# Performance work log

Measured on AMD Instinct MI355X. Metric: run time of the kernel, lower is better.

## Reference

```python
import jax, jax.numpy as jnp
import numpy as np

NUM_HEADS = 4


def setup_inputs() -> dict:
    key = jax.random.key(0)
    ks = jax.random.split(key, 5)
    B, N, D = 4096, 49, 128  # B = batch(64) * num_windows(64), N = 7*7 window
    nW = 64
    x = jax.random.normal(ks[0], (B, N, D), dtype=jnp.float32)
    mask = jax.random.normal(ks[1], (nW, N, N), dtype=jnp.float32)
    w_qkv = jax.random.normal(ks[2], (3 * D, D), dtype=jnp.float32) * 0.02
    w_proj = jax.random.normal(ks[3], (D, D), dtype=jnp.float32) * 0.02
    b_proj = jax.random.normal(ks[4], (D,), dtype=jnp.float32) * 0.02
    return {"x": x, "mask": mask, "w_qkv": w_qkv, "w_proj": w_proj, "b_proj": b_proj}


def reference(x, mask, w_qkv, w_proj, b_proj):
    B, N, D = x.shape
    H = NUM_HEADS
    hd = D // H
    scale = hd ** (-0.5)
    # qkv projection (torch Linear: y = x @ W^T), no bias
    qkv = (x @ w_qkv.T).reshape(B, N, 3, H, hd)
    qkv = jnp.transpose(qkv, (2, 0, 3, 1, 4))  # [3, B, H, N, hd]
    q, k, v = qkv[0], qkv[1], qkv[2]
    attn = jnp.einsum("bhqd,bhkd->bhqk", q, k) * scale  # [B, H, N, N]
    nW = mask.shape[0]
    # add per-window additive mask, broadcast over batch and heads
    attn = attn.reshape(B // nW, nW, H, N, N) + mask[None, :, None, :, :]
    attn = attn.reshape(B, H, N, N)
    attn = jax.nn.softmax(attn, axis=-1)
    out = jnp.einsum("bhqk,bhkd->bhqd", attn, v)  # [B, H, N, hd]
    out = jnp.transpose(out, (0, 2, 1, 3)).reshape(B, N, D)
    return out @ w_proj.T + b_proj
```

## Files before the change

kernel.cpp:

```cpp
#include <hip/hip_runtime.h>
#include <hip/hip_bf16.h>

typedef _Float16 f16;
typedef __attribute__((ext_vector_type(8))) _Float16 f16x8;
typedef __attribute__((ext_vector_type(4))) _Float16 f16x4;
typedef __attribute__((ext_vector_type(4))) float f32x4;

#define MFMA16(a, b, c) __builtin_amdgcn_mfma_f32_16x16x32_f16((a), (b), (c), 0, 0, 0)

#define NWIN 4096
#define WPB 16

__global__ void cvt_weights(const float* __restrict__ wq,
                            const float* __restrict__ wp,
                            f16* __restrict__ o) {
    int i = blockIdx.x * blockDim.x + threadIdx.x;
    if (i < 49152) o[i] = (f16)wq[i];
    if (i < 16384) o[49152 + i] = (f16)wp[i];
}

__device__ inline f16x8 cvt8(const float* p) {
    float4 u0 = *(const float4*)p;
    float4 u1 = *(const float4*)(p + 4);
    f16x8 t;
    t[0] = (f16)u0.x; t[1] = (f16)u0.y; t[2] = (f16)u0.z; t[3] = (f16)u0.w;
    t[4] = (f16)u1.x; t[5] = (f16)u1.y; t[6] = (f16)u1.z; t[7] = (f16)u1.w;
    return t;
}

__global__ __launch_bounds__(512, 1)
void fused_all(const float* __restrict__ x, const float* __restrict__ mask,
               const f16* __restrict__ wq_h, const f16* __restrict__ wp_h,
               const float* __restrict__ bias, float* __restrict__ out) {
    __shared__ f16 xb[2][50 * 128];
    __shared__ f16 qlds[2][64 * 128];
    __shared__ f16 klds[2][64 * 128];
    __shared__ f16 vlds[2][128 * 64];
    __shared__ f16 scr[8][2048];

    const int tid = threadIdx.x;
    const int wave = tid >> 6;
    const int lane = tid & 63;
    const int lg = lane >> 4;
    const int lr = lane & 15;
    const int w0 = blockIdx.x * WPB;

    const int amt = wave & 3;
    const int ahh = wave >> 2;
    const int ar0 = amt * 16;

    f16* ps0 = scr[wave];
    f16* ps1 = scr[wave] + 1024;

    f16x8 bw[3][4];
#pragma unroll
    for (int j = 0; j < 3; ++j)
#pragma unroll
        for (int kc = 0; kc < 4; ++kc)
            bw[j][kc] = *(const f16x8*)&wq_h[((wave + 8 * j) * 16 + lr) * 128 + kc * 32 + 8 * lg];
    f16x8 wpr[4];
#pragma unroll
    for (int kc = 0; kc < 4; ++kc)
        wpr[kc] = *(const f16x8*)&wp_h[(wave * 16 + lr) * 128 + kc * 32 + 8 * lg];
    const float4 bcv = *(const float4*)&bias[wave * 16 + 4 * lg];

    auto stage = [&](int w, int p) {
        const float* xw = x + (size_t)w * (49 * 128);
        for (int i = tid; i < 1568; i += 512) {
            const int row = i >> 5;
            const int c4 = (i & 31) << 2;
            float4 v = ((const float4*)xw)[i];
            f16x4 t;
            t[0] = (f16)v.x; t[1] = (f16)v.y; t[2] = (f16)v.z; t[3] = (f16)v.w;
            *(f16x4*)&xb[p][row * 128 + (c4 ^ ((row & 7) << 3))] = t;
        }
    };

    stage(w0, 0);
    __syncthreads();

    const float sc = 0.17677669529663687f;

    for (int wi = 0; wi < WPB; ++wi) {
        const int w = w0 + wi;
        const int cur = wi & 1;
        if (wi < WPB - 1) stage(w + 1, cur ^ 1);

        const float* mw = mask + (size_t)(w & 63) * (49 * 49);
        const int qrow = ar0 + lr;
        float mv[4][4];
#pragma unroll
        for (int reg = 0; reg < 4; ++reg) {
#pragma unroll
            for (int nt = 0; nt < 4; ++nt) {
                const int k = 4 * lg + reg + 16 * nt;
                mv[reg][nt] = (qrow < 49 && k < 49) ? mw[qrow * 49 + k] : 0.f;
            }
        }

        f16* ql = qlds[cur];
        f16* kl = klds[cur];
        f16* vl = vlds[cur];
#pragma unroll
        for (int mt = 0; mt < 4; ++mt) {
            const int nb = mt * 16;
            const int xrow = nb + lr;
            f16x8 a[4];
            if (xrow < 49) {
#pragma unroll
                for (int kc = 0; kc < 4; ++kc)
                    a[kc] = *(const f16x8*)&xb[cur][xrow * 128 + ((kc * 32 + 8 * lg) ^ ((xrow & 7) << 3))];
            } else {
                f16x8 z = {0, 0, 0, 0, 0, 0, 0, 0};
#pragma unroll
                for (int kc = 0; kc < 4; ++kc) a[kc] = z;
            }

#pragma unroll
            for (int j = 0; j < 2; ++j) {
                __builtin_amdgcn_s_setprio(1);
                f32x4 acc = {0.f, 0.f, 0.f, 0.f};
#pragma unroll
                for (int kc = 0; kc < 4; ++kc) acc = MFMA16(bw[j][kc], a[kc], acc);
                __builtin_amdgcn_s_setprio(0);

                const int n = nb + lr;
                const int cb = wave * 16 + 4 * lg;
                f16x4 t;
#pragma unroll
                for (int reg = 0; reg < 4; ++reg) t[reg] = (f16)acc[reg];
                f16* dst = (j == 0) ? ql : kl;
                *(f16x4*)&dst[n * 128 + (cb ^ ((n & 7) << 3))] = t;
            }
            {
                __builtin_amdgcn_s_setprio(1);
                f32x4 acc = {0.f, 0.f, 0.f, 0.f};
#pragma unroll
                for (int kc = 0; kc < 4; ++kc) acc = MFMA16(a[kc], bw[2][kc], acc);
                __builtin_amdgcn_s_setprio(0);

                const int c = wave * 16 + lr;
                f16x4 t;
#pragma unroll
                for (int reg = 0; reg < 4; ++reg) t[reg] = (f16)acc[reg];
                *(f16x4*)&vl[c * 64 + ((nb + 4 * lg) ^ ((c & 7) << 3))] = t;
            }
        }
        __syncthreads();

        const int h0 = 2 * ahh;
        const int h1 = 2 * ahh + 1;

        f16x8 aq0 = *(const f16x8*)&ql[qrow * 128 + ((h0 * 32 + 8 * lg) ^ ((qrow & 7) << 3))];
        f16x8 aq1 = *(const f16x8*)&ql[qrow * 128 + ((h1 * 32 + 8 * lg) ^ ((qrow & 7) << 3))];

        f32x4 s0[4], s1[4];
        {
            __builtin_amdgcn_s_setprio(1);
#pragma unroll
            for (int nt = 0; nt < 4; ++nt) {
                const int krow = nt * 16 + lr;
                f16x8 bk = *(const f16x8*)&kl[krow * 128 + ((h0 * 32 + 8 * lg) ^ ((krow & 7) << 3))];
                f32x4 z = {0.f, 0.f, 0.f, 0.f};
                s0[nt] = MFMA16(bk, aq0, z);
            }
#pragma unroll
            for (int nt = 0; nt < 4; ++nt) {
                const int krow = nt * 16 + lr;
                f16x8 bk = *(const f16x8*)&kl[krow * 128 + ((h1 * 32 + 8 * lg) ^ ((krow & 7) << 3))];
                f32x4 z = {0.f, 0.f, 0.f, 0.f};
                s1[nt] = MFMA16(bk, aq1, z);
            }
            __builtin_amdgcn_s_setprio(0);
        }

        float sum0 = 0.f, sum1 = 0.f;
#pragma unroll
        for (int nt = 0; nt < 4; ++nt) {
            f16x4 p0t, p1t;
#pragma unroll
            for (int reg = 0; reg < 4; ++reg) {
                const int k = 4 * lg + reg + 16 * nt;
                float e0 = (k < 49) ? __expf(s0[nt][reg] * sc + mv[reg][nt]) : 0.f;
                float e1 = (k < 49) ? __expf(s1[nt][reg] * sc + mv[reg][nt]) : 0.f;
                sum0 += e0;
                sum1 += e1;
                p0t[reg] = (f16)e0;
                p1t[reg] = (f16)e1;
            }
            const int off = lr * 64 + ((4 * lg + 16 * nt) ^ ((lr & 7) << 3));
            *(f16x4*)&ps0[off] = p0t;
            *(f16x4*)&ps1[off] = p1t;
        }
        sum0 += __shfl_xor(sum0, 16, 64);
        sum0 += __shfl_xor(sum0, 32, 64);
        sum1 += __shfl_xor(sum1, 16, 64);
        sum1 += __shfl_xor(sum1, 32, 64);
        const float inv0 = __fdividef(1.f, sum0);
        const float inv1 = __fdividef(1.f, sum1);

        f16x8 bv0[2][2], bv1[2][2];
#pragma unroll
        for (int nt = 0; nt < 2; ++nt)
#pragma unroll
            for (int kc = 0; kc < 2; ++kc) {
                const int vr0 = h0 * 32 + nt * 16 + lr;
                const int vr1 = h1 * 32 + nt * 16 + lr;
                bv0[nt][kc] = *(const f16x8*)&vl[vr0 * 64 + ((kc * 32 + 8 * lg) ^ ((vr0 & 7) << 3))];
                bv1[nt][kc] = *(const f16x8*)&vl[vr1 * 64 + ((kc * 32 + 8 * lg) ^ ((vr1 & 7) << 3))];
            }

        f16x8 ap0[2], ap1[2];
#pragma unroll
        for (int kc = 0; kc < 2; ++kc) {
            const int off = lr * 64 + ((kc * 32 + 8 * lg) ^ ((lr & 7) << 3));
            ap0[kc] = *(const f16x8*)&ps0[off];
            ap1[kc] = *(const f16x8*)&ps1[off];
        }
        f32x4 o00 = {0.f, 0.f, 0.f, 0.f}, o01 = {0.f, 0.f, 0.f, 0.f};
        f32x4 o10 = {0.f, 0.f, 0.f, 0.f}, o11 = {0.f, 0.f, 0.f, 0.f};
        __builtin_amdgcn_s_setprio(1);
#pragma unroll
        for (int kc = 0; kc < 2; ++kc) {
            o00 = MFMA16(bv0[0][kc], ap0[kc], o00);
            o01 = MFMA16(bv0[1][kc], ap0[kc], o01);
            o10 = MFMA16(bv1[0][kc], ap1[kc], o10);
            o11 = MFMA16(bv1[1][kc], ap1[kc], o11);
        }
        __builtin_amdgcn_s_setprio(0);

#pragma unroll
        for (int reg = 0; reg < 4; ++reg) {
            o00[reg] *= inv0;
            o01[reg] *= inv0;
            o10[reg] *= inv1;
            o11[reg] *= inv1;
        }

        {
            const int n = ar0 + lr;
            const int s = (n & 7) << 3;
            f16x4 t;
#pragma unroll
            for (int reg = 0; reg < 4; ++reg) t[reg] = (f16)o00[reg];
            *(f16x4*)&ql[n * 128 + ((h0 * 32 + 4 * lg) ^ s)] = t;
#pragma unroll
            for (int reg = 0; reg < 4; ++reg) t[reg] = (f16)o01[reg];
            *(f16x4*)&ql[n * 128 + ((h0 * 32 + 16 + 4 * lg) ^ s)] = t;
#pragma unroll
            for (int reg = 0; reg < 4; ++reg) t[reg] = (f16)o10[reg];
            *(f16x4*)&ql[n * 128 + ((h1 * 32 + 4 * lg) ^ s)] = t;
#pragma unroll
            for (int reg = 0; reg < 4; ++reg) t[reg] = (f16)o11[reg];
            *(f16x4*)&ql[n * 128 + ((h1 * 32 + 16 + 4 * lg) ^ s)] = t;
        }
        __syncthreads();

        float* ob = out + (size_t)w * (49 * 128);
#pragma unroll
        for (int mt = 0; mt < 4; ++mt) {
            const int prow = mt * 16 + lr;
            f16x8 aa[4];
#pragma unroll
            for (int kc = 0; kc < 4; ++kc)
                aa[kc] = *(const f16x8*)&ql[prow * 128 + ((kc * 32 + 8 * lg) ^ ((prow & 7) << 3))];
            __builtin_amdgcn_s_setprio(1);
            f32x4 acc = {0.f, 0.f, 0.f, 0.f};
#pragma unroll
            for (int kc = 0; kc < 4; ++kc) acc = MFMA16(wpr[kc], aa[kc], acc);
            __builtin_amdgcn_s_setprio(0);

            if (prow < 49) {
                float4 o;
                o.x = acc[0] + bcv.x;
                o.y = acc[1] + bcv.y;
                o.z = acc[2] + bcv.z;
                o.w = acc[3] + bcv.w;
                *(float4*)&ob[prow * 128 + wave * 16 + 4 * lg] = o;
            }
        }
    }
}

template <bool WB>
__global__ __launch_bounds__(256, 4)
void fused_wattn(const float* __restrict__ x, const float* __restrict__ mask,
                 const float* __restrict__ wq_f, const float* __restrict__ wp_f,
                 const f16* __restrict__ wq_h, const f16* __restrict__ wp_h,
                 const float* __restrict__ bias, float* __restrict__ out) {
    __shared__ f16 ks[64 * 128];
    __shared__ f16 vt[128 * 64];
    __shared__ f16 scr[4][1024];

    const int b = blockIdx.x;
    const int wid = b & 63;
    const int tid = threadIdx.x;
    const int wave = tid >> 6;
    const int lane = tid & 63;
    const int lg = lane >> 4;
    const int lr = lane & 15;
    const int r0 = wave * 16;
    f16* ps = scr[wave];

    f16x8 a[4];
    {
        const int xrow = r0 + lr;
        if (xrow < 49) {
            const float* xp = x + ((size_t)b * 49 + xrow) * 128 + 8 * lg;
#pragma unroll
            for (int kc = 0; kc < 4; ++kc) a[kc] = cvt8(xp + kc * 32);
        } else {
            f16x8 z = {0, 0, 0, 0, 0, 0, 0, 0};
#pragma unroll
            for (int kc = 0; kc < 4; ++kc) a[kc] = z;
        }
    }

    float mv[4][4];
#pragma unroll
    for (int reg = 0; reg < 4; ++reg) {
        const int n = r0 + 4 * lg + reg;
#pragma unroll
        for (int nt = 0; nt < 4; ++nt) {
            const int col = nt * 16 + lr;
            mv[reg][nt] = (n < 49 && col < 49) ? mask[((size_t)wid * 49 + n) * 49 + col] : 0.f;
        }
    }

    f16x4 qd[8];
#pragma unroll
    for (int ct = 0; ct < 24; ++ct) {
        const int wrow = ct * 16 + lr;
        f16x8 bw[4];
        if (WB) {
#pragma unroll
            for (int kc = 0; kc < 4; ++kc)
                bw[kc] = *(const f16x8*)&wq_h[wrow * 128 + kc * 32 + 8 * lg];
        } else {
#pragma unroll
            for (int kc = 0; kc < 4; ++kc)
                bw[kc] = cvt8(&wq_f[wrow * 128 + kc * 32 + 8 * lg]);
        }
        f32x4 acc = {0.f, 0.f, 0.f, 0.f};
#pragma unroll
        for (int kc = 0; kc < 4; ++kc) acc = MFMA16(a[kc], bw[kc], acc);

        if (ct < 8) {
            f16x4 q;
#pragma unroll
            for (int reg = 0; reg < 4; ++reg) q[reg] = (f16)acc[reg];
            qd[ct] = q;
        } else if (ct < 16) {
#pragma unroll
            for (int reg = 0; reg < 4; ++reg) {
                const int n = r0 + 4 * lg + reg;
                const int c = wrow - 128;
                ks[n * 128 + (c ^ ((n & 7) << 3))] = (f16)acc[reg];
            }
        } else {
#pragma unroll
            for (int reg = 0; reg < 4; ++reg) {
                const int n = r0 + 4 * lg + reg;
                const int dch = wrow - 256;
                vt[dch * 64 + (n ^ ((dch & 7) << 3))] = (f16)acc[reg];
            }
        }
    }
    __syncthreads();

    const float sc = 0.17677669529663687f;
    f32x4 oacc[4][2];

#pragma unroll
    for (int h = 0; h < 4; ++h) {
#pragma unroll
        for (int c2 = 0; c2 < 2; ++c2)
#pragma unroll
            for (int reg = 0; reg < 4; ++reg) {
                const int row = 4 * lg + reg;
                const int col = c2 * 16 + lr;
                ps[row * 32 + (col ^ ((row & 3) << 3))] = qd[2 * h + c2][reg];
            }
        f16x8 aq = *(const f16x8*)&ps[lr * 32 + ((8 * lg) ^ ((lr & 3) << 3))];

        f32x4 s[4];
#pragma unroll
        for (int nt = 0; nt < 4; ++nt) {
            const int krow = nt * 16 + lr;
            f16x8 bk = *(const f16x8*)&ks[krow * 128 + ((h * 32 + 8 * lg) ^ ((krow & 7) << 3))];
            f32x4 z = {0.f, 0.f, 0.f, 0.f};
            s[nt] = MFMA16(aq, bk, z);
        }

#pragma unroll
        for (int reg = 0; reg < 4; ++reg) {
            float vals[4];
            float sum = 0.f;
#pragma unroll
            for (int nt = 0; nt < 4; ++nt) {
                const int col = nt * 16 + lr;
                float e = (col < 49) ? __expf(s[nt][reg] * sc + mv[reg][nt]) : 0.f;
                vals[nt] = e;
                sum += e;
            }
            for (int d = 1; d < 16; d <<= 1) sum += __shfl_xor(sum, d, 64);
            const float inv = __fdividef(1.f, sum);
            const int row = 4 * lg + reg;
#pragma unroll
            for (int nt = 0; nt < 4; ++nt) {
                const int col = nt * 16 + lr;
                ps[row * 64 + (col ^ ((row & 7) << 3))] = (f16)(vals[nt] * inv);
            }
        }

        f16x8 ap[2];
#pragma unroll
        for (int kc = 0; kc < 2; ++kc)
            ap[kc] = *(const f16x8*)&ps[lr * 64 + ((kc * 32 + 8 * lg) ^ ((lr & 7) << 3))];
#pragma unroll
        for (int nt = 0; nt < 2; ++nt) {
            const int vrow = h * 32 + nt * 16 + lr;
            f32x4 acc = {0.f, 0.f, 0.f, 0.f};
#pragma unroll
            for (int kc = 0; kc < 2; ++kc) {
                f16x8 bv = *(const f16x8*)&vt[vrow * 64 + ((kc * 32 + 8 * lg) ^ ((vrow & 7) << 3))];
                acc = MFMA16(ap[kc], bv, acc);
            }
            oacc[h][nt] = acc;
        }
    }

    f16x8 aa[4];
#pragma unroll
    for (int pass = 0; pass < 2; ++pass) {
#pragma unroll
        for (int h2 = 0; h2 < 2; ++h2)
#pragma unroll
            for (int nt = 0; nt < 2; ++nt)
#pragma unroll
                for (int reg = 0; reg < 4; ++reg) {
                    const int row = 4 * lg + reg;
                    const int col = h2 * 32 + nt * 16 + lr;
                    ps[row * 64 + (col ^ ((row & 7) << 3))] = (f16)oacc[pass * 2 + h2][nt][reg];
                }
#pragma unroll
        for (int kcg = 0; kcg < 2; ++kcg)
            aa[pass * 2 + kcg] = *(const f16x8*)&ps[lr * 64 + ((kcg * 32 + 8 * lg) ^ ((lr & 7) << 3))];
    }

    float* ob = out + (size_t)b * (49 * 128);
#pragma unroll
    for (int ct = 0; ct < 8; ++ct) {
        const int wrow = ct * 16 + lr;
        f16x8 bw[4];
        if (WB) {
#pragma unroll
            for (int kc = 0; kc < 4; ++kc)
                bw[kc] = *(const f16x8*)&wp_h[wrow * 128 + kc * 32 + 8 * lg];
        } else {
#pragma unroll
            for (int kc = 0; kc < 4; ++kc)
                bw[kc] = cvt8(&wp_f[wrow * 128 + kc * 32 + 8 * lg]);
        }
        f32x4 acc = {0.f, 0.f, 0.f, 0.f};
#pragma unroll
        for (int kc = 0; kc < 4; ++kc) acc = MFMA16(aa[kc], bw[kc], acc);

        const float bc = bias[wrow];
#pragma unroll
        for (int reg = 0; reg < 4; ++reg) {
            const int n = r0 + 4 * lg + reg;
            if (n < 49) ob[n * 128 + ct * 16 + lr] = acc[reg] + bc;
        }
    }
}

extern "C" void kernel_launch(void* const* d_in, const int* in_sizes, int n_in,
                              void* d_out, int out_size, void* d_ws, size_t ws_size,
                              hipStream_t stream) {
    const float* x = (const float*)d_in[0];
    const float* mask = (const float*)d_in[1];
    const float* wq = (const float*)d_in[2];
    const float* wp = (const float*)d_in[3];
    const float* bp = (const float*)d_in[4];
    float* out = (float*)d_out;

    const size_t need_wb = (size_t)(49152 + 16384) * sizeof(f16);

    if (ws_size >= need_wb && d_ws != nullptr) {
        f16* wsh = (f16*)d_ws;
        cvt_weights<<<192, 256, 0, stream>>>(wq, wp, wsh);
        fused_all<<<NWIN / WPB, 512, 0, stream>>>(x, mask, wsh, wsh + 49152, bp, out);
    } else {
        fused_wattn<false><<<4096, 256, 0, stream>>>(x, mask, wq, wp, nullptr, nullptr, bp, out);
    }
}
```

Baseline: 98.11 us.

## Split 1024-thread block into two halves processing interleaved windows concurrently

The fused attention kernel now runs 1024 threads per block as two independent 512-thread halves, each owning one of the previously double-buffered LDS sets and processing alternating windows. This replaces the old software prefetch (stage next window into the other buffer) with staging issued after the QKV sync, and the per-head attention is processed sequentially to shrink register pressure and scratch. The aim is more resident waves to hide latency, at the cost of block-wide barriers coupling both halves and an extra barrier per iteration.

```diff
diff --git a/kernel.cpp b/kernel.cpp
--- a/kernel.cpp
+++ b/kernel.cpp
@@ -9,7 +9,7 @@
 #define MFMA16(a, b, c) __builtin_amdgcn_mfma_f32_16x16x32_f16((a), (b), (c), 0, 0, 0)
 
 #define NWIN 4096
-#define WPB 16
+#define WPH 8
 
 __global__ void cvt_weights(const float* __restrict__ wq,
                             const float* __restrict__ wp,
@@ -28,7 +28,7 @@
     return t;
 }
 
-__global__ __launch_bounds__(512, 1)
+__global__ __launch_bounds__(1024, 1)
 void fused_all(const float* __restrict__ x, const float* __restrict__ mask,
                const f16* __restrict__ wq_h, const f16* __restrict__ wp_h,
                const float* __restrict__ bias, float* __restrict__ out) {
@@ -36,55 +36,55 @@
     __shared__ f16 qlds[2][64 * 128];
     __shared__ f16 klds[2][64 * 128];
     __shared__ f16 vlds[2][128 * 64];
-    __shared__ f16 scr[8][2048];
+    __shared__ f16 scr[16][1024];
 
     const int tid = threadIdx.x;
     const int wave = tid >> 6;
+    const int half = wave >> 3;
+    const int hw = wave & 7;
+    const int ltid = tid & 511;
     const int lane = tid & 63;
     const int lg = lane >> 4;
     const int lr = lane & 15;
-    const int w0 = blockIdx.x * WPB;
-
-    const int amt = wave & 3;
-    const int ahh = wave >> 2;
+    const int w0 = blockIdx.x * (2 * WPH);
+
+    const int amt = hw & 3;
+    const int ahh = hw >> 2;
     const int ar0 = amt * 16;
 
-    f16* ps0 = scr[wave];
-    f16* ps1 = scr[wave] + 1024;
+    f16* ps = scr[wave];
 
     f16x8 bw[3][4];
 #pragma unroll
     for (int j = 0; j < 3; ++j)
 #pragma unroll
         for (int kc = 0; kc < 4; ++kc)
-            bw[j][kc] = *(const f16x8*)&wq_h[((wave + 8 * j) * 16 + lr) * 128 + kc * 32 + 8 * lg];
+            bw[j][kc] = *(const f16x8*)&wq_h[((hw + 8 * j) * 16 + lr) * 128 + kc * 32 + 8 * lg];
     f16x8 wpr[4];
 #pragma unroll
     for (int kc = 0; kc < 4; ++kc)
-        wpr[kc] = *(const f16x8*)&wp_h[(wave * 16 + lr) * 128 + kc * 32 + 8 * lg];
-    const float4 bcv = *(const float4*)&bias[wave * 16 + 4 * lg];
-
-    auto stage = [&](int w, int p) {
+        wpr[kc] = *(const f16x8*)&wp_h[(hw * 16 + lr) * 128 + kc * 32 + 8 * lg];
+    const float4 bcv = *(const float4*)&bias[hw * 16 + 4 * lg];
+
+    auto stage = [&](int w) {
         const float* xw = x + (size_t)w * (49 * 128);
-        for (int i = tid; i < 1568; i += 512) {
+        for (int i = ltid; i < 1568; i += 512) {
             const int row = i >> 5;
             const int c4 = (i & 31) << 2;
             float4 v = ((const float4*)xw)[i];
             f16x4 t;
             t[0] = (f16)v.x; t[1] = (f16)v.y; t[2] = (f16)v.z; t[3] = (f16)v.w;
-            *(f16x4*)&xb[p][row * 128 + (c4 ^ ((row & 7) << 3))] = t;
+            *(f16x4*)&xb[half][row * 128 + (c4 ^ ((row & 7) << 3))] = t;
         }
     };
 
-    stage(w0, 0);
+    stage(w0 + half);
     __syncthreads();
 
     const float sc = 0.17677669529663687f;
 
-    for (int wi = 0; wi < WPB; ++wi) {
-        const int w = w0 + wi;
-        const int cur = wi & 1;
-        if (wi < WPB - 1) stage(w + 1, cur ^ 1);
+    for (int wi = 0; wi < WPH; ++wi) {
+        const int w = w0 + 2 * wi + half;
 
         const float* mw = mask + (size_t)(w & 63) * (49 * 49);
         const int qrow = ar0 + lr;
@@ -98,9 +98,9 @@
             }
         }
 
-        f16* ql = qlds[cur];
-        f16* kl = klds[cur];
-        f16* vl = vlds[cur];
+        f16* ql = qlds[half];
+        f16* kl = klds[half];
+        f16* vl = vlds[half];
 #pragma unroll
         for (int mt = 0; mt < 4; ++mt) {
             const int nb = mt * 16;
@@ -109,7 +109,7 @@
             if (xrow < 49) {
 #pragma unroll
                 for (int kc = 0; kc < 4; ++kc)
-                    a[kc] = *(const f16x8*)&xb[cur][xrow * 128 + ((kc * 32 + 8 * lg) ^ ((xrow & 7) << 3))];
+                    a[kc] = *(const f16x8*)&xb[half][xrow * 128 + ((kc * 32 + 8 * lg) ^ ((xrow & 7) << 3))];
             } else {
                 f16x8 z = {0, 0, 0, 0, 0, 0, 0, 0};
 #pragma unroll
@@ -125,7 +125,7 @@
                 __builtin_amdgcn_s_setprio(0);
 
                 const int n = nb + lr;
-                const int cb = wave * 16 + 4 * lg;
+                const int cb = hw * 16 + 4 * lg;
                 f16x4 t;
 #pragma unroll
                 for (int reg = 0; reg < 4; ++reg) t[reg] = (f16)acc[reg];
@@ -139,7 +139,7 @@
                 for (int kc = 0; kc < 4; ++kc) acc = MFMA16(a[kc], bw[2][kc], acc);
                 __builtin_amdgcn_s_setprio(0);
 
-                const int c = wave * 16 + lr;
+                const int c = hw * 16 + lr;
                 f16x4 t;
 #pragma unroll
                 for (int reg = 0; reg < 4; ++reg) t[reg] = (f16)acc[reg];
@@ -148,96 +148,85 @@
         }
         __syncthreads();
 
-        const int h0 = 2 * ahh;
-        const int h1 = 2 * ahh + 1;
-
-        f16x8 aq0 = *(const f16x8*)&ql[qrow * 128 + ((h0 * 32 + 8 * lg) ^ ((qrow & 7) << 3))];
-        f16x8 aq1 = *(const f16x8*)&ql[qrow * 128 + ((h1 * 32 + 8 * lg) ^ ((qrow & 7) << 3))];
-
-        f32x4 s0[4], s1[4];
-        {
+        if (wi + 1 < WPH) stage(w + 2);
+
+        f32x4 o00, o01, o10, o11;
+#pragma unroll
+        for (int hi = 0; hi < 2; ++hi) {
+            const int h = 2 * ahh + hi;
+            f16x8 aq = *(const f16x8*)&ql[qrow * 128 + ((h * 32 + 8 * lg) ^ ((qrow & 7) << 3))];
+
+            f32x4 s[4];
             __builtin_amdgcn_s_setprio(1);
 #pragma unroll
             for (int nt = 0; nt < 4; ++nt) {
                 const int krow = nt * 16 + lr;
-                f16x8 bk = *(const f16x8*)&kl[krow * 128 + ((h0 * 32 + 8 * lg) ^ ((krow & 7) << 3))];
+                f16x8 bk = *(const f16x8*)&kl[krow * 128 + ((h * 32 + 8 * lg) ^ ((krow & 7) << 3))];
                 f32x4 z = {0.f, 0.f, 0.f, 0.f};
-                s0[nt] = MFMA16(bk, aq0, z);
-            }
+                s[nt] = MFMA16(bk, aq, z);
+            }
+            __builtin_amdgcn_s_setprio(0);
+
+            float sum = 0.f;
 #pragma unroll
             for (int nt = 0; nt < 4; ++nt) {
-                const int krow = nt * 16 + lr;
-                f16x8 bk = *(const f16x8*)&kl[krow * 128 + ((h1 * 32 + 8 * lg) ^ ((krow & 7) << 3))];
-                f32x4 z = {0.f, 0.f, 0.f, 0.f};
-                s1[nt] = MFMA16(bk, aq1, z);
+                f16x4 pt;
+#pragma unroll
+                for (int reg = 0; reg < 4; ++reg) {
+                    const int k = 4 * lg + reg + 16 * nt;
+                    float e = (k < 49) ? __expf(s[nt][reg] * sc + mv[reg][nt]) : 0.f;
+                    sum += e;
+                    pt[reg] = (f16)e;
+                }
+                const int off = lr * 64 + ((4 * lg + 16 * nt) ^ ((lr & 7) << 3));
+                *(f16x4*)&ps[off] = pt;
+            }
+            sum += __shfl_xor(sum, 16, 64);
+            sum += __shfl_xor(sum, 32, 64);
+            const float inv = __fdividef(1.f, sum);
+
+            f16x8 bv[2][2];
+#pragma unroll
+            for (int nt = 0; nt < 2; ++nt)
+#pragma unroll
+                for (int kc = 0; kc < 2; ++kc) {
+                    const int vr = h * 32 + nt * 16 + lr;
+                    bv[nt][kc] = *(const f16x8*)&vl[vr * 64 + ((kc * 32 + 8 * lg) ^ ((vr & 7) << 3))];
+                }
+
+            f16x8 ap[2];
+#pragma unroll
+            for (int kc = 0; kc < 2; ++kc) {
+                const int off = lr * 64 + ((kc * 32 + 8 * lg) ^ ((lr & 7) << 3));
+                ap[kc] = *(const f16x8*)&ps[off];
+            }
+            f32x4 oa = {0.f, 0.f, 0.f, 0.f};
+            f32x4 ob_ = {0.f, 0.f, 0.f, 0.f};
+            __builtin_amdgcn_s_setprio(1);
+#pragma unroll
+            for (int kc = 0; kc < 2; ++kc) {
+                oa = MFMA16(bv[0][kc], ap[kc], oa);
+                ob_ = MFMA16(bv[1][kc], ap[kc], ob_);
             }
             __builtin_amdgcn_s_setprio(0);
-        }
-
-        float sum0 = 0.f, sum1 = 0.f;
-#pragma unroll
-        for (int nt = 0; nt < 4; ++nt) {
-            f16x4 p0t, p1t;
+
 #pragma unroll
             for (int reg = 0; reg < 4; ++reg) {
-                const int k = 4 * lg + reg + 16 * nt;
-                float e0 = (k < 49) ? __expf(s0[nt][reg] * sc + mv[reg][nt]) : 0.f;
-                float e1 = (k < 49) ? __expf(s1[nt][reg] * sc + mv[reg][nt]) : 0.f;
-                sum0 += e0;
-                sum1 += e1;
-                p0t[reg] = (f16)e0;
-                p1t[reg] = (f16)e1;
-            }
-            const int off = lr * 64 + ((4 * lg + 16 * nt) ^ ((lr & 7) << 3));
-            *(f16x4*)&ps0[off] = p0t;
-            *(f16x4*)&ps1[off] = p1t;
-        }
-        sum0 += __shfl_xor(sum0, 16, 64);
-        sum0 += __shfl_xor(sum0, 32, 64);
-        sum1 += __shfl_xor(sum1, 16, 64);
-        sum1 += __shfl_xor(sum1, 32, 64);
-        const float inv0 = __fdividef(1.f, sum0);
-        const float inv1 = __fdividef(1.f, sum1);
-
-        f16x8 bv0[2][2], bv1[2][2];
-#pragma unroll
-        for (int nt = 0; nt < 2; ++nt)
-#pragma unroll
-            for (int kc = 0; kc < 2; ++kc) {
-                const int vr0 = h0 * 32 + nt * 16 + lr;
-                const int vr1 = h1 * 32 + nt * 16 + lr;
-                bv0[nt][kc] = *(const f16x8*)&vl[vr0 * 64 + ((kc * 32 + 8 * lg) ^ ((vr0 & 7) << 3))];
-                bv1[nt][kc] = *(const f16x8*)&vl[vr1 * 64 + ((kc * 32 + 8 * lg) ^ ((vr1 & 7) << 3))];
-            }
-
-        f16x8 ap0[2], ap1[2];
-#pragma unroll
-        for (int kc = 0; kc < 2; ++kc) {
-            const int off = lr * 64 + ((kc * 32 + 8 * lg) ^ ((lr & 7) << 3));
-            ap0[kc] = *(const f16x8*)&ps0[off];
-            ap1[kc] = *(const f16x8*)&ps1[off];
-        }
-        f32x4 o00 = {0.f, 0.f, 0.f, 0.f}, o01 = {0.f, 0.f, 0.f, 0.f};
-        f32x4 o10 = {0.f, 0.f, 0.f, 0.f}, o11 = {0.f, 0.f, 0.f, 0.f};
-        __builtin_amdgcn_s_setprio(1);
-#pragma unroll
-        for (int kc = 0; kc < 2; ++kc) {
-            o00 = MFMA16(bv0[0][kc], ap0[kc], o00);
-            o01 = MFMA16(bv0[1][kc], ap0[kc], o01);
-            o10 = MFMA16(bv1[0][kc], ap1[kc], o10);
-            o11 = MFMA16(bv1[1][kc], ap1[kc], o11);
-        }
-        __builtin_amdgcn_s_setprio(0);
-
-#pragma unroll
-        for (int reg = 0; reg < 4; ++reg) {
-            o00[reg] *= inv0;
-            o01[reg] *= inv0;
-            o10[reg] *= inv1;
-            o11[reg] *= inv1;
+                oa[reg] *= inv;
+                ob_[reg] *= inv;
+            }
+            if (hi == 0) {
+                o00 = oa;
+                o01 = ob_;
+            } else {
+                o10 = oa;
+                o11 = ob_;
+            }
         }
 
         {
+            const int h0 = 2 * ahh;
+            const int h1 = 2 * ahh + 1;
             const int n = ar0 + lr;
             const int s = (n & 7) << 3;
             f16x4 t;
@@ -276,9 +265,10 @@
                 o.y = acc[1] + bcv.y;
                 o.z = acc[2] + bcv.z;
                 o.w = acc[3] + bcv.w;
-                *(float4*)&ob[prow * 128 + wave * 16 + 4 * lg] = o;
-            }
-        }
+                *(float4*)&ob[prow * 128 + hw * 16 + 4 * lg] = o;
+            }
+        }
+        __syncthreads();
     }
 }
 
@@ -490,7 +480,7 @@
     if (ws_size >= need_wb && d_ws != nullptr) {
         f16* wsh = (f16*)d_ws;
         cvt_weights<<<192, 256, 0, stream>>>(wq, wp, wsh);
-        fused_all<<<NWIN / WPB, 512, 0, stream>>>(x, mask, wsh, wsh + 49152, bp, out);
+        fused_all<<<NWIN / (2 * WPH), 1024, 0, stream>>>(x, mask, wsh, wsh + 49152, bp, out);
     } else {
         fused_wattn<false><<<4096, 256, 0, stream>>>(x, mask, wq, wp, nullptr, nullptr, bp, out);
     }
```

Measured after the change: 217.9 us. 122% more time.

## Process windows in pairs per phase to halve block barriers

Applied to the files above, without the earlier changes.

The persistent kernel now handles two windows per iteration. It runs QKV projection for both, syncs, stages the next two windows' x, runs attention for both, syncs, then runs the output projection for both. This cuts barriers per window and lets more independent work sit between them. It also replaces the per-element k<49 select in the softmax with a -1e30 mask bias. In exchange, prefetch of x is now serialized after the first barrier rather than overlapped with QKV, and a third barrier per pair is added.

```diff
diff --git a/kernel.cpp b/kernel.cpp
--- a/kernel.cpp
+++ b/kernel.cpp
@@ -48,6 +48,7 @@
     const int amt = wave & 3;
     const int ahh = wave >> 2;
     const int ar0 = amt * 16;
+    const int qrow = ar0 + lr;
 
     f16* ps0 = scr[wave];
     f16* ps1 = scr[wave] + 1024;
@@ -77,85 +78,98 @@
     };
 
     stage(w0, 0);
+    stage(w0 + 1, 1);
     __syncthreads();
 
     const float sc = 0.17677669529663687f;
 
-    for (int wi = 0; wi < WPB; ++wi) {
-        const int w = w0 + wi;
-        const int cur = wi & 1;
-        if (wi < WPB - 1) stage(w + 1, cur ^ 1);
-
-        const float* mw = mask + (size_t)(w & 63) * (49 * 49);
-        const int qrow = ar0 + lr;
-        float mv[4][4];
-#pragma unroll
-        for (int reg = 0; reg < 4; ++reg) {
-#pragma unroll
-            for (int nt = 0; nt < 4; ++nt) {
-                const int k = 4 * lg + reg + 16 * nt;
-                mv[reg][nt] = (qrow < 49 && k < 49) ? mw[qrow * 49 + k] : 0.f;
-            }
-        }
-
-        f16* ql = qlds[cur];
-        f16* kl = klds[cur];
-        f16* vl = vlds[cur];
-#pragma unroll
-        for (int mt = 0; mt < 4; ++mt) {
-            const int nb = mt * 16;
-            const int xrow = nb + lr;
-            f16x8 a[4];
-            if (xrow < 49) {
-#pragma unroll
-                for (int kc = 0; kc < 4; ++kc)
-                    a[kc] = *(const f16x8*)&xb[cur][xrow * 128 + ((kc * 32 + 8 * lg) ^ ((xrow & 7) << 3))];
-            } else {
-                f16x8 z = {0, 0, 0, 0, 0, 0, 0, 0};
-#pragma unroll
-                for (int kc = 0; kc < 4; ++kc) a[kc] = z;
-            }
-
-#pragma unroll
-            for (int j = 0; j < 2; ++j) {
-                __builtin_amdgcn_s_setprio(1);
-                f32x4 acc = {0.f, 0.f, 0.f, 0.f};
-#pragma unroll
-                for (int kc = 0; kc < 4; ++kc) acc = MFMA16(bw[j][kc], a[kc], acc);
-                __builtin_amdgcn_s_setprio(0);
-
-                const int n = nb + lr;
-                const int cb = wave * 16 + 4 * lg;
-                f16x4 t;
-#pragma unroll
-                for (int reg = 0; reg < 4; ++reg) t[reg] = (f16)acc[reg];
-                f16* dst = (j == 0) ? ql : kl;
-                *(f16x4*)&dst[n * 128 + (cb ^ ((n & 7) << 3))] = t;
-            }
-            {
-                __builtin_amdgcn_s_setprio(1);
-                f32x4 acc = {0.f, 0.f, 0.f, 0.f};
-#pragma unroll
-                for (int kc = 0; kc < 4; ++kc) acc = MFMA16(a[kc], bw[2][kc], acc);
-                __builtin_amdgcn_s_setprio(0);
-
-                const int c = wave * 16 + lr;
-                f16x4 t;
-#pragma unroll
-                for (int reg = 0; reg < 4; ++reg) t[reg] = (f16)acc[reg];
-                *(f16x4*)&vl[c * 64 + ((nb + 4 * lg) ^ ((c & 7) << 3))] = t;
+    for (int pi = 0; pi < WPB / 2; ++pi) {
+        const int wA = w0 + 2 * pi;
+
+#pragma unroll
+        for (int ws = 0; ws < 2; ++ws) {
+            f16* ql = qlds[ws];
+            f16* kl = klds[ws];
+            f16* vl = vlds[ws];
+#pragma unroll
+            for (int mt = 0; mt < 4; ++mt) {
+                const int nb = mt * 16;
+                const int xrow = nb + lr;
+                f16x8 a[4];
+                if (xrow < 49) {
+#pragma unroll
+                    for (int kc = 0; kc < 4; ++kc)
+                        a[kc] = *(const f16x8*)&xb[ws][xrow * 128 + ((kc * 32 + 8 * lg) ^ ((xrow & 7) << 3))];
+                } else {
+                    f16x8 z = {0, 0, 0, 0, 0, 0, 0, 0};
+#pragma unroll
+                    for (int kc = 0; kc < 4; ++kc) a[kc] = z;
+                }
+
+#pragma unroll
+                for (int j = 0; j < 2; ++j) {
+                    __builtin_amdgcn_s_setprio(1);
+                    f32x4 acc = {0.f, 0.f, 0.f, 0.f};
+#pragma unroll
+                    for (int kc = 0; kc < 4; ++kc) acc = MFMA16(bw[j][kc], a[kc], acc);
+                    __builtin_amdgcn_s_setprio(0);
+
+                    const int n = nb + lr;
+                    const int cb = wave * 16 + 4 * lg;
+                    f16x4 t;
+#pragma unroll
+                    for (int reg = 0; reg < 4; ++reg) t[reg] = (f16)acc[reg];
+                    f16* dst = (j == 0) ? ql : kl;
+                    *(f16x4*)&dst[n * 128 + (cb ^ ((n & 7) << 3))] = t;
+                }
+                {
+                    __builtin_amdgcn_s_setprio(1);
+                    f32x4 acc = {0.f, 0.f, 0.f, 0.f};
+#pragma unroll
+                    for (int kc = 0; kc < 4; ++kc) acc = MFMA16(a[kc], bw[2][kc], acc);
+                    __builtin_amdgcn_s_setprio(0);
+
+                    const int c = wave * 16 + lr;
+                    f16x4 t;
+#pragma unroll
+                    for (int reg = 0; reg < 4; ++reg) t[reg] = (f16)acc[reg];
+                    *(f16x4*)&vl[c * 64 + ((nb + 4 * lg) ^ ((c & 7) << 3))] = t;
+                }
             }
         }
         __syncthreads();
 
-        const int h0 = 2 * ahh;
-        const int h1 = 2 * ahh + 1;
-
-        f16x8 aq0 = *(const f16x8*)&ql[qrow * 128 + ((h0 * 32 + 8 * lg) ^ ((qrow & 7) << 3))];
-        f16x8 aq1 = *(const f16x8*)&ql[qrow * 128 + ((h1 * 32 + 8 * lg) ^ ((qrow & 7) << 3))];
-
-        f32x4 s0[4], s1[4];
-        {
+        if (pi + 1 < WPB / 2) {
+            stage(wA + 2, 0);
+            stage(wA + 3, 1);
+        }
+
+#pragma unroll
+        for (int ws = 0; ws < 2; ++ws) {
+            const int w = wA + ws;
+            f16* ql = qlds[ws];
+            f16* kl = klds[ws];
+            f16* vl = vlds[ws];
+
+            const int h0 = 2 * ahh;
+            const int h1 = 2 * ahh + 1;
+
+            const float* mw = mask + (size_t)(w & 63) * (49 * 49);
+            float mv[4][4];
+#pragma unroll
+            for (int reg = 0; reg < 4; ++reg) {
+#pragma unroll
+                for (int nt = 0; nt < 4; ++nt) {
+                    const int k = 4 * lg + reg + 16 * nt;
+                    mv[reg][nt] = (k >= 49) ? -1e30f
+                                  : (qrow < 49) ? mw[qrow * 49 + k] : 0.f;
+                }
+            }
+
+            f16x8 aq0 = *(const f16x8*)&ql[qrow * 128 + ((h0 * 32 + 8 * lg) ^ ((qrow & 7) << 3))];
+            f16x8 aq1 = *(const f16x8*)&ql[qrow * 128 + ((h1 * 32 + 8 * lg) ^ ((qrow & 7) << 3))];
+
+            f32x4 s0[4], s1[4];
             __builtin_amdgcn_s_setprio(1);
 #pragma unroll
             for (int nt = 0; nt < 4; ++nt) {
@@ -172,113 +186,109 @@
                 s1[nt] = MFMA16(bk, aq1, z);
             }
             __builtin_amdgcn_s_setprio(0);
-        }
-
-        float sum0 = 0.f, sum1 = 0.f;
-#pragma unroll
-        for (int nt = 0; nt < 4; ++nt) {
-            f16x4 p0t, p1t;
-#pragma unroll
-            for (int reg = 0; reg < 4; ++reg) {
-                const int k = 4 * lg + reg + 16 * nt;
-                float e0 = (k < 49) ? __expf(s0[nt][reg] * sc + mv[reg][nt]) : 0.f;
-                float e1 = (k < 49) ? __expf(s1[nt][reg] * sc + mv[reg][nt]) : 0.f;
-                sum0 += e0;
-                sum1 += e1;
-                p0t[reg] = (f16)e0;
-                p1t[reg] = (f16)e1;
-            }
-            const int off = lr * 64 + ((4 * lg + 16 * nt) ^ ((lr & 7) << 3));
-            *(f16x4*)&ps0[off] = p0t;
-            *(f16x4*)&ps1[off] = p1t;
-        }
-        sum0 += __shfl_xor(sum0, 16, 64);
-        sum0 += __shfl_xor(sum0, 32, 64);
-        sum1 += __shfl_xor(sum1, 16, 64);
-        sum1 += __shfl_xor(sum1, 32, 64);
-        const float inv0 = __fdividef(1.f, sum0);
-        const float inv1 = __fdividef(1.f, sum1);
-
-        f16x8 bv0[2][2], bv1[2][2];
-#pragma unroll
-        for (int nt = 0; nt < 2; ++nt)
+
+            float sum0 = 0.f, sum1 = 0.f;
+#pragma unroll
+            for (int nt = 0; nt < 4; ++nt) {
+                f16x4 p0t, p1t;
+#pragma unroll
+                for (int reg = 0; reg < 4; ++reg) {
+                    float e0 = __expf(s0[nt][reg] * sc + mv[reg][nt]);
+                    float e1 = __expf(s1[nt][reg] * sc + mv[reg][nt]);
+                    sum0 += e0;
+                    sum1 += e1;
+                    p0t[reg] = (f16)e0;
+                    p1t[reg] = (f16)e1;
+                }
+                const int off = lr * 64 + ((4 * lg + 16 * nt) ^ ((lr & 7) << 3));
+                *(f16x4*)&ps0[off] = p0t;
+                *(f16x4*)&ps1[off] = p1t;
+            }
+            sum0 += __shfl_xor(sum0, 16, 64);
+            sum0 += __shfl_xor(sum0, 32, 64);
+            sum1 += __shfl_xor(sum1, 16, 64);
+            sum1 += __shfl_xor(sum1, 32, 64);
+            const float inv0 = __fdividef(1.f, sum0);
+            const float inv1 = __fdividef(1.f, sum1);
+
+            f16x8 bv0[2][2], bv1[2][2];
+#pragma unroll
+            for (int nt = 0; nt < 2; ++nt)
+#pragma unroll
+                for (int kc = 0; kc < 2; ++kc) {
+                    const int vr0 = h0 * 32 + nt * 16 + lr;
+                    const int vr1 = h1 * 32 + nt * 16 + lr;
+                    bv0[nt][kc] = *(const f16x8*)&vl[vr0 * 64 + ((kc * 32 + 8 * lg) ^ ((vr0 & 7) << 3))];
+                    bv1[nt][kc] = *(const f16x8*)&vl[vr1 * 64 + ((kc * 32 + 8 * lg) ^ ((vr1 & 7) << 3))];
+                }
+
+            f16x8 ap0[2], ap1[2];
 #pragma unroll
             for (int kc = 0; kc < 2; ++kc) {
-                const int vr0 = h0 * 32 + nt * 16 + lr;
-                const int vr1 = h1 * 32 + nt * 16 + lr;
-                bv0[nt][kc] = *(const f16x8*)&vl[vr0 * 64 + ((kc * 32 + 8 * lg) ^ ((vr0 & 7) << 3))];
-                bv1[nt][kc] = *(const f16x8*)&vl[vr1 * 64 + ((kc * 32 + 8 * lg) ^ ((vr1 & 7) << 3))];
-            }
-
-        f16x8 ap0[2], ap1[2];
-#pragma unroll
-        for (int kc = 0; kc < 2; ++kc) {
-            const int off = lr * 64 + ((kc * 32 + 8 * lg) ^ ((lr & 7) << 3));
-            ap0[kc] = *(const f16x8*)&ps0[off];
-            ap1[kc] = *(const f16x8*)&ps1[off];
-        }
-        f32x4 o00 = {0.f, 0.f, 0.f, 0.f}, o01 = {0.f, 0.f, 0.f, 0.f};
-        f32x4 o10 = {0.f, 0.f, 0.f, 0.f}, o11 = {0.f, 0.f, 0.f, 0.f};
-        __builtin_amdgcn_s_setprio(1);
-#pragma unroll
-        for (int kc = 0; kc < 2; ++kc) {
-            o00 = MFMA16(bv0[0][kc], ap0[kc], o00);
-            o01 = MFMA16(bv0[1][kc], ap0[kc], o01);
-            o10 = MFMA16(bv1[0][kc], ap1[kc], o10);
-            o11 = MFMA16(bv1[1][kc], ap1[kc], o11);
-        }
-        __builtin_amdgcn_s_setprio(0);
-
-#pragma unroll
-        for (int reg = 0; reg < 4; ++reg) {
-            o00[reg] *= inv0;
-            o01[reg] *= inv0;
-            o10[reg] *= inv1;
-            o11[reg] *= inv1;
-        }
-
-        {
-            const int n = ar0 + lr;
-            const int s = (n & 7) << 3;
-            f16x4 t;
-#pragma unroll
-            for (int reg = 0; reg < 4; ++reg) t[reg] = (f16)o00[reg];
-            *(f16x4*)&ql[n * 128 + ((h0 * 32 + 4 * lg) ^ s)] = t;
-#pragma unroll
-            for (int reg = 0; reg < 4; ++reg) t[reg] = (f16)o01[reg];
-            *(f16x4*)&ql[n * 128 + ((h0 * 32 + 16 + 4 * lg) ^ s)] = t;
-#pragma unroll
-            for (int reg = 0; reg < 4; ++reg) t[reg] = (f16)o10[reg];
-            *(f16x4*)&ql[n * 128 + ((h1 * 32 + 4 * lg) ^ s)] = t;
-#pragma unroll
-            for (int reg = 0; reg < 4; ++reg) t[reg] = (f16)o11[reg];
-            *(f16x4*)&ql[n * 128 + ((h1 * 32 + 16 + 4 * lg) ^ s)] = t;
+                const int off = lr * 64 + ((kc * 32 + 8 * lg) ^ ((lr & 7) << 3));
+                ap0[kc] = *(const f16x8*)&ps0[off];
+                ap1[kc] = *(const f16x8*)&ps1[off];
+            }
+            f32x4 o00 = {0.f, 0.f, 0.f, 0.f}, o01 = {0.f, 0.f, 0.f, 0.f};
+            f32x4 o10 = {0.f, 0.f, 0.f, 0.f}, o11 = {0.f, 0.f, 0.f, 0.f};
+            __builtin_amdgcn_s_setprio(1);
+#pragma unroll
+            for (int kc = 0; kc < 2; ++kc) {
+                o00 = MFMA16(bv0[0][kc], ap0[kc], o00);
+                o01 = MFMA16(bv0[1][kc], ap0[kc], o01);
+                o10 = MFMA16(bv1[0][kc], ap1[kc], o10);
+                o11 = MFMA16(bv1[1][kc], ap1[kc], o11);
+            }
+            __builtin_amdgcn_s_setprio(0);
+
+            {
+                const int n = ar0 + lr;
+                const int s = (n & 7) << 3;
+                f16x4 t;
+#pragma unroll
+                for (int reg = 0; reg < 4; ++reg) t[reg] = (f16)(o00[reg] * inv0);
+                *(f16x4*)&ql[n * 128 + ((h0 * 32 + 4 * lg) ^ s)] = t;
+#pragma unroll
+                for (int reg = 0; reg < 4; ++reg) t[reg] = (f16)(o01[reg] * inv0);
+                *(f16x4*)&ql[n * 128 + ((h0 * 32 + 16 + 4 * lg) ^ s)] = t;
+#pragma unroll
+                for (int reg = 0; reg < 4; ++reg) t[reg] = (f16)(o10[reg] * inv1);
+                *(f16x4*)&ql[n * 128 + ((h1 * 32 + 4 * lg) ^ s)] = t;
+#pragma unroll
+                for (int reg = 0; reg < 4; ++reg) t[reg] = (f16)(o11[reg] * inv1);
+                *(f16x4*)&ql[n * 128 + ((h1 * 32 + 16 + 4 * lg) ^ s)] = t;
+            }
         }
         __syncthreads();
 
-        float* ob = out + (size_t)w * (49 * 128);
-#pragma unroll
-        for (int mt = 0; mt < 4; ++mt) {
-            const int prow = mt * 16 + lr;
-            f16x8 aa[4];
-#pragma unroll
-            for (int kc = 0; kc < 4; ++kc)
-                aa[kc] = *(const f16x8*)&ql[prow * 128 + ((kc * 32 + 8 * lg) ^ ((prow & 7) << 3))];
-            __builtin_amdgcn_s_setprio(1);
-            f32x4 acc = {0.f, 0.f, 0.f, 0.f};
-#pragma unroll
-            for (int kc = 0; kc < 4; ++kc) acc = MFMA16(wpr[kc], aa[kc], acc);
-            __builtin_amdgcn_s_setprio(0);
-
-            if (prow < 49) {
-                float4 o;
-                o.x = acc[0] + bcv.x;
-                o.y = acc[1] + bcv.y;
-                o.z = acc[2] + bcv.z;
-                o.w = acc[3] + bcv.w;
-                *(float4*)&ob[prow * 128 + wave * 16 + 4 * lg] = o;
-            }
-        }
+#pragma unroll
+        for (int ws = 0; ws < 2; ++ws) {
+            const f16* ql = qlds[ws];
+            float* ob = out + (size_t)(wA + ws) * (49 * 128);
+#pragma unroll
+            for (int mt = 0; mt < 4; ++mt) {
+                const int prow = mt * 16 + lr;
+                f16x8 aa[4];
+#pragma unroll
+                for (int kc = 0; kc < 4; ++kc)
+                    aa[kc] = *(const f16x8*)&ql[prow * 128 + ((kc * 32 + 8 * lg) ^ ((prow & 7) << 3))];
+                __builtin_amdgcn_s_setprio(1);
+                f32x4 acc = {0.f, 0.f, 0.f, 0.f};
+#pragma unroll
+                for (int kc = 0; kc < 4; ++kc) acc = MFMA16(wpr[kc], aa[kc], acc);
+                __builtin_amdgcn_s_setprio(0);
+
+                if (prow < 49) {
+                    float4 o;
+                    o.x = acc[0] + bcv.x;
+                    o.y = acc[1] + bcv.y;
+                    o.z = acc[2] + bcv.z;
+                    o.w = acc[3] + bcv.w;
+                    *(float4*)&ob[prow * 128 + wave * 16 + 4 * lg] = o;
+                }
+            }
+        }
+        __syncthreads();
     }
 }
 
```

Measured after the change: 90.95 us, median of 2. 1.08x faster.
